# Optimization experiments

Measured on AMD Instinct MI355X. Metric: run time of the kernel, lower is better.

## Reference

```python
import jax, jax.numpy as jnp
import numpy as np

N, E, G, H = 25000, 400000, 64, 8


def setup_inputs() -> dict:
    key = jax.random.key(0)
    ks = iter(jax.random.split(key, 64))
    nrm = lambda *s: jax.random.normal(next(ks), s, dtype=jnp.float32) * 0.1
    inp = {}
    inp['x'] = jax.random.normal(next(ks), (N, 3), dtype=jnp.float32)
    inp['edge_index'] = jax.random.randint(next(ks), (2, E), 0, N)
    inp['edge_attr'] = jax.random.uniform(next(ks), (E, 1), dtype=jnp.float32)
    inp['batch'] = jnp.sort(jax.random.randint(next(ks), (N,), 0, G))
    inp['inbn_g'] = jnp.ones(3, jnp.float32); inp['inbn_b'] = jnp.zeros(3, jnp.float32)
    # GAT layer 0: in=3, heads=8, C=8, concat -> 64
    inp['w0'] = nrm(3, 64); inp['we0'] = nrm(1, 64)
    inp['as0'] = nrm(8, 8); inp['ad0'] = nrm(8, 8); inp['ae0'] = nrm(8, 8)
    inp['b0'] = jnp.zeros(64, jnp.float32)
    inp['bng0'] = jnp.ones(64, jnp.float32); inp['bnb0'] = jnp.zeros(64, jnp.float32)
    # GAT layer 1: in=64, heads=8, C=8, concat -> 64
    inp['w1'] = nrm(64, 64); inp['we1'] = nrm(1, 64)
    inp['as1'] = nrm(8, 8); inp['ad1'] = nrm(8, 8); inp['ae1'] = nrm(8, 8)
    inp['b1'] = jnp.zeros(64, jnp.float32)
    inp['bng1'] = jnp.ones(64, jnp.float32); inp['bnb1'] = jnp.zeros(64, jnp.float32)
    # GAT layer 2: in=64, heads=8, C=64, concat=False (mean over heads) -> 64
    inp['w2'] = nrm(64, 512); inp['we2'] = nrm(1, 512)
    inp['as2'] = nrm(8, 64); inp['ad2'] = nrm(8, 64); inp['ae2'] = nrm(8, 64)
    inp['b2'] = jnp.zeros(64, jnp.float32)
    inp['bng2'] = jnp.ones(64, jnp.float32); inp['bnb2'] = jnp.zeros(64, jnp.float32)
    # MLP head (weights stored [in, out])
    inp['fc1_w'] = nrm(128, 128); inp['fc1_b'] = jnp.zeros(128, jnp.float32)
    inp['fc2_w'] = nrm(128, 64); inp['fc2_b'] = jnp.zeros(64, jnp.float32)
    inp['fg_w'] = nrm(64, 1); inp['fg_b'] = jnp.zeros(1, jnp.float32)
    inp['fb_w'] = nrm(64, 1); inp['fb_b'] = jnp.zeros(1, jnp.float32)
    return inp


def _bn(x, g, b):
    # training-mode batch norm over node dim (biased variance)
    m = x.mean(0)
    v = jnp.mean((x - m) ** 2, 0)
    return (x - m) * jax.lax.rsqrt(v + 1e-5) * g + b


def _gat(x, ei, ea, W, We, a_s, a_d, a_e, bias, concat):
    n = x.shape[0]
    h, c = a_s.shape
    xs = (x @ W).reshape(n, h, c)                       # [N,H,C]
    asrc = jnp.einsum('nhc,hc->nh', xs, a_s)            # [N,H]
    adst = jnp.einsum('nhc,hc->nh', xs, a_d)
    ee = (ea @ We).reshape(-1, h, c)                    # [E,H,C]
    aedge = jnp.einsum('ehc,hc->eh', ee, a_e)           # [E,H]
    s, d = ei[0], ei[1]
    logit = jax.nn.leaky_relu(asrc[s] + adst[d] + aedge, 0.2)   # [E,H]
    # segment softmax over incoming edges of each destination node
    mx = jax.ops.segment_max(logit, d, num_segments=n)
    mx = jnp.where(jnp.isfinite(mx), mx, 0.0)
    ez = jnp.exp(logit - mx[d])
    den = jax.ops.segment_sum(ez, d, num_segments=n)
    alpha = ez / jnp.maximum(den[d], 1e-16)             # [E,H]
    out = jax.ops.segment_sum(alpha[:, :, None] * xs[s], d, num_segments=n)  # [N,H,C]
    out = out.reshape(n, h * c) if concat else out.mean(1)
    return out + bias


def reference(x, edge_index, edge_attr, batch, inbn_g, inbn_b,
              w0, we0, as0, ad0, ae0, b0, bng0, bnb0,
              w1, we1, as1, ad1, ae1, b1, bng1, bnb1,
              w2, we2, as2, ad2, ae2, b2, bng2, bnb2,
              fc1_w, fc1_b, fc2_w, fc2_b, fg_w, fg_b, fb_w, fb_b):
    x = _bn(x, inbn_g, inbn_b)
    # layer 0 (no residual: 3 != 64)
    x = jax.nn.elu(_bn(_gat(x, edge_index, edge_attr, w0, we0, as0, ad0, ae0, b0, True), bng0, bnb0))
    # layer 1 (residual)
    x = x + jax.nn.elu(_bn(_gat(x, edge_index, edge_attr, w1, we1, as1, ad1, ae1, b1, True), bng1, bnb1))
    # layer 2 (concat=False, residual)
    x = x + jax.nn.elu(_bn(_gat(x, edge_index, edge_attr, w2, we2, as2, ad2, ae2, b2, False), bng2, bnb2))
    # dual pooling per graph
    cnt = jax.ops.segment_sum(jnp.ones((x.shape[0],), x.dtype), batch, num_segments=G)
    x_mean = jax.ops.segment_sum(x, batch, num_segments=G) / jnp.maximum(cnt, 1.0)[:, None]
    x_max = jax.ops.segment_max(x, batch, num_segments=G)
    g = jnp.concatenate([x_mean, x_max], axis=1)        # [G,128]
    g = jax.nn.elu(g @ fc1_w + fc1_b)
    g = jax.nn.elu(g @ fc2_w + fc2_b)
    gamma = g @ fg_w + fg_b
    beta = g @ fb_w + fb_b
    return jnp.concatenate([gamma, beta], axis=1)       # [G, 2*p_layers]
```

## Files before the change

### kernel.cpp

```cpp
#include <hip/hip_runtime.h>
#include <math.h>

#define NN 25000
#define EE 400000
#define GG 64

static const int O_DEG   = 0;
static const int ZERO_END= 25000;
static const int O_ROWS  = 25008;
static const int O_CUR   = 50016;
static const int O_GOFF  = 75016;
static const int O_IPART = 75088;
static const int O_INBN  = 75184;
static const int O_WS    = 75192;
static const int O_WD    = 76728;
static const int O_WE    = 78264;
static const int O_BPART = 78288;
static const int O_AB    = 94672;
static const int O_BSW   = 94800;
static const int O_CSRC  = 111184;
static const int O_CEA   = 511184;
static const int O_XS    = 911184;
static const int O_ASRC  = 2511184;
static const int O_ADST  = 2711184;
static const int O_AGG   = 2911184;
static const int O_X     = 4511184;
static const int O_BSWC  = 6111184;
static const int O_BSWA  = 6113744;
static const int O_BSUM  = 6114256;
static const int O_BOFF  = 6114360;

using f32x4 = __attribute__((ext_vector_type(4))) float;
using sh8   = __attribute__((ext_vector_type(8))) short;

__device__ inline short f2bf(float f) {
    unsigned u = __float_as_uint(f);
    unsigned r = (u + 0x7FFFu + ((u >> 16) & 1u)) >> 16;
    return (short)r;
}

__global__ void k_pre(const int* __restrict__ ei, const int* __restrict__ batch,
                      const float* __restrict__ x3,
                      const float* w0, const float* we0, const float* as0, const float* ad0, const float* ae0,
                      const float* w1, const float* we1, const float* as1, const float* ad1, const float* ae1,
                      const float* w2, const float* we2, const float* as2, const float* ad2, const float* ae2,
                      int* __restrict__ deg, int* __restrict__ goff, float* __restrict__ ipart,
                      float* __restrict__ Ws, float* __restrict__ Wd, float* __restrict__ wev,
                      short* __restrict__ bsw, short* __restrict__ bswc, short* __restrict__ bswa) {
    __shared__ float sd[1536];
    int b = blockIdx.x, t = threadIdx.x;
    if (b < 1563) {
        int e = b * 256 + t;
        if (e < EE) atomicAdd(&deg[ei[EE + e]], 1);
    } else if (b < 1579) {
        int ib = b - 1563;
        float s[3] = {0,0,0}, q[3] = {0,0,0};
        for (int n = ib * 256 + t; n < NN; n += 16 * 256) {
#pragma unroll
            for (int i = 0; i < 3; i++) { float v = x3[n*3+i]; s[i] += v; q[i] += v*v; }
        }
#pragma unroll
        for (int i = 0; i < 3; i++) { sd[t*6+i] = s[i]; sd[t*6+3+i] = q[i]; }
        __syncthreads();
        for (int off = 128; off > 0; off >>= 1) {
            if (t < off) {
#pragma unroll
                for (int i = 0; i < 6; i++) sd[t*6+i] += sd[(t+off)*6+i];
            }
            __syncthreads();
        }
        if (t < 6) ipart[ib*6 + t] = sd[t];
    } else if (b == 1579) {
        if (t <= GG) {
            int g = t, lo = 0, hi = NN;
            while (lo < hi) { int mid = (lo + hi) >> 1; if (batch[mid] < g) lo = mid + 1; else hi = mid; }
            goff[g] = lo;
        }
    } else if (b < 1583) {
        int L = b - 1580;
        const float *W, *Wep, *as_, *ad_, *ae_; int INF, CC;
        if (L == 0)      { W = w0; Wep = we0; as_ = as0; ad_ = ad0; ae_ = ae0; INF = 3;  CC = 8;  }
        else if (L == 1) { W = w1; Wep = we1; as_ = as1; ad_ = ad1; ae_ = ae1; INF = 64; CC = 8;  }
        else             { W = w2; Wep = we2; as_ = as2; ad_ = ad2; ae_ = ae2; INF = 64; CC = 64; }
        int HC = 8 * CC;
        for (int tt = t; tt < INF * 8; tt += 256) {
            int i = tt >> 3, h = tt & 7;
            float s = 0.f, d = 0.f;
            for (int c = 0; c < CC; c++) {
                float w = W[i*HC + h*CC + c];
                s += w * as_[h*CC + c];
                d += w * ad_[h*CC + c];
            }
            Ws[L*512 + i*8 + h] = s; Wd[L*512 + i*8 + h] = d;
        }
        if (t < 8) {
            float s = 0.f;
            for (int c = 0; c < CC; c++) s += Wep[t*CC + c] * ae_[t*CC + c];
            wev[L*8 + t] = s;
        }
    } else if (b < 1711) {
        int idx = (b - 1583) * 256 + t;
        int j  = idx & 7;
        int l  = (idx >> 3) & 63;
        int nt = (idx >> 9) & 3;
        int kb = idx >> 11;
        int k = kb*32 + (l >> 4)*4 + (j & 3) + 16*(j >> 2);
        int c = nt*16 + (l & 15);
        int h = k >> 6, i = k & 63;
        bsw[idx] = f2bf(w2[i*512 + h*64 + c]);
    } else if (b < 1731) {
        int idx = (b - 1711) * 256 + t;
        int j  = idx & 7;
        int l  = (idx >> 3) & 63;
        int r2 = idx >> 9;
        int nt = r2 % 5, kb = r2 / 5;
        int k = kb*32 + (l >> 4)*4 + (j & 3) + 16*(j >> 2);
        int c = nt*16 + (l & 15);
        float val;
        if (c < 64) val = w1[k*64 + c];
        else {
            int h = (c - 64) & 7;
            const float* aa = (c < 72) ? as1 : ad1;
            float s = 0.f;
            for (int cc = 0; cc < 8; cc++) s += w1[k*64 + h*8 + cc] * aa[h*8 + cc];
            val = s;
        }
        bswc[idx] = f2bf(val);
    } else {
        int idx = (b - 1731) * 256 + t;
        int j  = idx & 7;
        int l  = (idx >> 3) & 63;
        int kb = idx >> 9;
        int k = kb*32 + (l >> 4)*4 + (j & 3) + 16*(j >> 2);
        int c = l & 15;
        int h = c & 7;
        const float* aa = (c < 8) ? as2 : ad2;
        float s = 0.f;
        for (int cc = 0; cc < 64; cc++) s += w2[k*512 + h*64 + cc] * aa[h*64 + cc];
        bswa[idx] = f2bf(s);
    }
}

__global__ void k_scan1(const int* __restrict__ deg, int* __restrict__ rows,
                        int* __restrict__ bsum) {
    int t = threadIdx.x, b = blockIdx.x;
    int i = b * 256 + t;
    int v = (i < NN) ? deg[i] : 0;
    __shared__ int sd[256];
    sd[t] = v; __syncthreads();
    for (int off = 1; off < 256; off <<= 1) {
        int x = (t >= off) ? sd[t - off] : 0;
        __syncthreads();
        sd[t] += x;
        __syncthreads();
    }
    if (i < NN) rows[i] = sd[t] - v;
    if (t == 255) bsum[b] = sd[255];
}

__global__ void k_scan2(const int* __restrict__ bsum, int* __restrict__ boff,
                        const float* __restrict__ ipart, float* __restrict__ inbn) {
    int t = threadIdx.x;
    if (t == 0) {
        int run = 0;
        for (int b = 0; b < 98; b++) { int v = bsum[b]; boff[b] = run; run += v; }
    }
    if (t < 6) { float s = 0.f; for (int b = 0; b < 16; b++) s += ipart[b*6 + t]; inbn[t] = s; }
}

__global__ void k_scan3(const int* __restrict__ boff, int* __restrict__ rows,
                        int* __restrict__ cur) {
    int t = threadIdx.x, b = blockIdx.x;
    int i = b * 256 + t;
    if (i < NN) {
        int r = rows[i] + boff[b];
        rows[i] = r;
        cur[i] = r;
    }
    if (b == 0 && t == 0) rows[NN] = EE;
}

__global__ void k_fill(const int* __restrict__ ei, const float* __restrict__ ea,
                       int* __restrict__ cur, int* __restrict__ csrc,
                       float* __restrict__ cea) {
    int e = blockIdx.x * 256 + threadIdx.x;
    if (e >= EE) return;
    int s = ei[e], d = ei[EE + e];
    int pos = atomicAdd(&cur[d], 1);
    csrc[pos] = s; cea[pos] = ea[e];
}

__global__ void k_proj0(const float* __restrict__ x, const float* __restrict__ sums,
                        const float* __restrict__ g, const float* __restrict__ b,
                        const float* __restrict__ W0,
                        const float* __restrict__ Ws, const float* __restrict__ Wd,
                        float* __restrict__ xs, float* __restrict__ asrc, float* __restrict__ adst) {
    int idx = blockIdx.x * 256 + threadIdx.x;
    if (idx >= NN * 64) return;
    int n = idx >> 6, j = idx & 63;
    float xn[3];
#pragma unroll
    for (int i = 0; i < 3; i++) {
        float m = sums[i] * (1.0f / NN);
        float v = sums[3+i] * (1.0f / NN) - m*m;
        xn[i] = (x[n*3+i] - m) * rsqrtf(v + 1e-5f) * g[i] + b[i];
    }
    float a = 0.f;
#pragma unroll
    for (int i = 0; i < 3; i++) a += xn[i] * W0[i*64 + j];
    xs[n*64 + j] = a;
    if (j < 16) {
        const float* WA = (j < 8) ? Ws : Wd;
        int h = j & 7;
        float s = 0.f;
#pragma unroll
        for (int i = 0; i < 3; i++) s += xn[i] * WA[i*8 + h];
        if (j < 8) asrc[n*8 + h] = s; else adst[n*8 + h] = s;
    }
}

__global__ void k_agg8f(const int* __restrict__ rows, const int* __restrict__ csrc,
                        const float* __restrict__ cea,
                        const float* __restrict__ asrc, const float* __restrict__ adst,
                        const float* __restrict__ wev,
                        const float* __restrict__ xs, float* __restrict__ agg) {
    int lane = threadIdx.x & 63;
    int d = (blockIdx.x * blockDim.x + threadIdx.x) >> 6;
    if (d >= NN) return;
    int h = lane >> 3;
    float adh = adst[d*8 + h];
    float wh  = wev[h];
    int rs = rows[d], re = rows[d+1];
    float acc = 0.f, den = 0.f;
    for (int c0 = rs; c0 < re; c0 += 64) {
        int cnt = re - c0; if (cnt > 64) cnt = 64;
        int ii = c0 + (lane < cnt ? lane : 0);
        int es = csrc[ii];
        float ef = cea[ii];
        int j = 0;
        for (; j + 3 < cnt; j += 4) {
            int s0 = __shfl(es, j),   s1 = __shfl(es, j+1);
            int s2 = __shfl(es, j+2), s3 = __shfl(es, j+3);
            float a0 = __shfl(ef, j),   a1 = __shfl(ef, j+1);
            float a2 = __shfl(ef, j+2), a3 = __shfl(ef, j+3);
            float l0 = asrc[s0*8+h], l1 = asrc[s1*8+h];
            float l2 = asrc[s2*8+h], l3 = asrc[s3*8+h];
            float x0 = xs[s0*64+lane], x1 = xs[s1*64+lane];
            float x2 = xs[s2*64+lane], x3 = xs[s3*64+lane];
            l0 += adh + a0*wh; l1 += adh + a1*wh;
            l2 += adh + a2*wh; l3 += adh + a3*wh;
            l0 = fmaxf(l0, 0.2f*l0); l1 = fmaxf(l1, 0.2f*l1);
            l2 = fmaxf(l2, 0.2f*l2); l3 = fmaxf(l3, 0.2f*l3);
            float e0 = __expf(l0), e1 = __expf(l1), e2 = __expf(l2), e3 = __expf(l3);
            den += (e0 + e1) + (e2 + e3);
            acc += e0*x0; acc += e1*x1; acc += e2*x2; acc += e3*x3;
        }
        for (; j < cnt; j++) {
            int s = __shfl(es, j);
            float a = __shfl(ef, j);
            float l = asrc[s*8+h] + adh + a*wh;
            l = fmaxf(l, 0.2f*l);
            float e = __expf(l);
            den += e;
            acc += e * xs[s*64+lane];
        }
    }
    agg[d*64 + lane] = acc / fmaxf(den, 1e-16f);
}

__global__ void k_proj1m(const float* __restrict__ agg, const float* __restrict__ ab,
                         const short* __restrict__ bswc,
                         float* __restrict__ xb, float* __restrict__ xs,
                         float* __restrict__ asrc, float* __restrict__ adst) {
    int l = threadIdx.x & 63;
    int wid = (blockIdx.x * blockDim.x + threadIdx.x) >> 6;
    int n0 = wid * 16;
    if (n0 >= NN) return;
    int ra = n0 + (l & 15); if (ra > NN-1) ra = NN-1;
    int kq = (l >> 4) * 4;
    const sh8* Bs = (const sh8*)bswc;
    sh8 af0, af1;
#pragma unroll
    for (int kb = 0; kb < 2; kb++) {
        int c0 = kb*32 + kq;
        float4 a0 = *(const float4*)&agg[ra*64 + c0];
        float4 a1 = *(const float4*)&agg[ra*64 + c0 + 16];
        float4 sc0 = *(const float4*)&ab[c0];
        float4 sh0 = *(const float4*)&ab[64 + c0];
        float4 sc1 = *(const float4*)&ab[c0 + 16];
        float4 sh1 = *(const float4*)&ab[64 + c0 + 16];
        float o[8];
        o[0] = a0.x*sc0.x + sh0.x; o[1] = a0.y*sc0.y + sh0.y;
        o[2] = a0.z*sc0.z + sh0.z; o[3] = a0.w*sc0.w + sh0.w;
        o[4] = a1.x*sc1.x + sh1.x; o[5] = a1.y*sc1.y + sh1.y;
        o[6] = a1.z*sc1.z + sh1.z; o[7] = a1.w*sc1.w + sh1.w;
#pragma unroll
        for (int u = 0; u < 8; u++) o[u] = (o[u] > 0.f) ? o[u] : (__expf(o[u]) - 1.f);
        float4 w0v = {o[0],o[1],o[2],o[3]}, w1v = {o[4],o[5],o[6],o[7]};
        *(float4*)&xb[ra*64 + c0]      = w0v;
        *(float4*)&xb[ra*64 + c0 + 16] = w1v;
        sh8 af;
#pragma unroll
        for (int u = 0; u < 8; u++) af[u] = f2bf(o[u]);
        if (kb == 0) af0 = af; else af1 = af;
    }
    f32x4 acc[5];
#pragma unroll
    for (int nt = 0; nt < 5; nt++) acc[nt] = (f32x4){0,0,0,0};
#pragma unroll
    for (int nt = 0; nt < 5; nt++) {
        acc[nt] = __builtin_amdgcn_mfma_f32_16x16x32_bf16(af0, Bs[nt*64 + l], acc[nt], 0, 0, 0);
        acc[nt] = __builtin_amdgcn_mfma_f32_16x16x32_bf16(af1, Bs[(5+nt)*64 + l], acc[nt], 0, 0, 0);
    }
    int rbase = n0 + (l >> 4) * 4, cb = l & 15;
#pragma unroll
    for (int r = 0; r < 4; r++) {
        int n = rbase + r;
        if (n >= NN) break;
#pragma unroll
        for (int nt = 0; nt < 4; nt++) xs[n*64 + nt*16 + cb] = acc[nt][r];
        if (cb < 8) asrc[n*8 + cb] = acc[4][r];
        else        adst[n*8 + (cb-8)] = acc[4][r];
    }
}

__global__ void k_bnattn(const float* __restrict__ agg, const float* __restrict__ ab,
                         const short* __restrict__ bswa,
                         float* __restrict__ xb,
                         float* __restrict__ asrc, float* __restrict__ adst) {
    int l = threadIdx.x & 63;
    int wid = (blockIdx.x * blockDim.x + threadIdx.x) >> 6;
    int n0 = wid * 16;
    if (n0 >= NN) return;
    int ra = n0 + (l & 15); if (ra > NN-1) ra = NN-1;
    int kq = (l >> 4) * 4;
    const sh8* Bs = (const sh8*)bswa;
    sh8 af0, af1;
#pragma unroll
    for (int kb = 0; kb < 2; kb++) {
        int c0 = kb*32 + kq;
        float4 a0 = *(const float4*)&agg[ra*64 + c0];
        float4 a1 = *(const float4*)&agg[ra*64 + c0 + 16];
        float4 x0 = *(const float4*)&xb[ra*64 + c0];
        float4 x1 = *(const float4*)&xb[ra*64 + c0 + 16];
        float4 sc0 = *(const float4*)&ab[c0];
        float4 sh0 = *(const float4*)&ab[64 + c0];
        float4 sc1 = *(const float4*)&ab[c0 + 16];
        float4 sh1 = *(const float4*)&ab[64 + c0 + 16];
        float o[8];
        o[0] = a0.x*sc0.x + sh0.x; o[1] = a0.y*sc0.y + sh0.y;
        o[2] = a0.z*sc0.z + sh0.z; o[3] = a0.w*sc0.w + sh0.w;
        o[4] = a1.x*sc1.x + sh1.x; o[5] = a1.y*sc1.y + sh1.y;
        o[6] = a1.z*sc1.z + sh1.z; o[7] = a1.w*sc1.w + sh1.w;
#pragma unroll
        for (int u = 0; u < 8; u++) o[u] = (o[u] > 0.f) ? o[u] : (__expf(o[u]) - 1.f);
        o[0] += x0.x; o[1] += x0.y; o[2] += x0.z; o[3] += x0.w;
        o[4] += x1.x; o[5] += x1.y; o[6] += x1.z; o[7] += x1.w;
        float4 w0v = {o[0],o[1],o[2],o[3]}, w1v = {o[4],o[5],o[6],o[7]};
        *(float4*)&xb[ra*64 + c0]      = w0v;
        *(float4*)&xb[ra*64 + c0 + 16] = w1v;
        sh8 af;
#pragma unroll
        for (int u = 0; u < 8; u++) af[u] = f2bf(o[u]);
        if (kb == 0) af0 = af; else af1 = af;
    }
    f32x4 acc = {0,0,0,0};
    acc = __builtin_amdgcn_mfma_f32_16x16x32_bf16(af0, Bs[l],      acc, 0, 0, 0);
    acc = __builtin_amdgcn_mfma_f32_16x16x32_bf16(af1, Bs[64 + l], acc, 0, 0, 0);
    int rbase = n0 + (l >> 4) * 4, cb = l & 15;
#pragma unroll
    for (int r = 0; r < 4; r++) {
        int n = rbase + r;
        if (n >= NN) break;
        if (cb < 8) asrc[n*8 + cb] = acc[r];
        else        adst[n*8 + (cb-8)] = acc[r];
    }
}

__global__ __launch_bounds__(256) void k_l2f(
        const int* __restrict__ rows, const int* __restrict__ csrc,
        const float* __restrict__ cea,
        const float* __restrict__ asrc, const float* __restrict__ adst,
        const float* __restrict__ wev,
        const float* __restrict__ x, const short* __restrict__ bsw,
        float* __restrict__ agg) {
    __shared__ short zl[16 * 520];
    int t = threadIdx.x, lane = t & 63, wv = t >> 6;
    int blk = blockIdx.x;
    int h = lane >> 3;
    float wh = wev[h];
    const float4* x4 = (const float4*)x;
    int fo   = (lane & 7) * 2;
    int kb_w = lane >> 2;
    int qd0  = 2 * (lane & 1);
    int jhi  = 4 * ((lane >> 1) & 1);
    for (int q = 0; q < 4; q++) {
        int r = wv * 4 + q;
        int d = blk * 16 + r;
        float acc[8] = {0,0,0,0,0,0,0,0};
        float den = 0.f;
        if (d < NN) {
            float adh = adst[d*8 + h];
            int rs = rows[d], re = rows[d+1];
            for (int c0 = rs; c0 < re; c0 += 64) {
                int cnt = re - c0; if (cnt > 64) cnt = 64;
                int ii = c0 + (lane < cnt ? lane : 0);
                int es = csrc[ii];
                float ef = cea[ii];
                int j = 0;
                for (; j + 1 < cnt; j += 2) {
                    int s0 = __shfl(es, j), s1 = __shfl(es, j+1);
                    float a0 = __shfl(ef, j), a1 = __shfl(ef, j+1);
                    float l0 = asrc[s0*8+h], l1 = asrc[s1*8+h];
                    float4 u0 = x4[s0*16 + fo], u1 = x4[s0*16 + fo + 1];
                    float4 v0 = x4[s1*16 + fo], v1 = x4[s1*16 + fo + 1];
                    l0 += adh + a0*wh; l1 += adh + a1*wh;
                    l0 = fmaxf(l0, 0.2f*l0); l1 = fmaxf(l1, 0.2f*l1);
                    float e0 = __expf(l0), e1 = __expf(l1);
                    den += e0 + e1;
                    acc[0] += e0*u0.x + e1*v0.x;
                    acc[1] += e0*u0.y + e1*v0.y;
                    acc[2] += e0*u0.z + e1*v0.z;
                    acc[3] += e0*u0.w + e1*v0.w;
                    acc[4] += e0*u1.x + e1*v1.x;
                    acc[5] += e0*u1.y + e1*v1.y;
                    acc[6] += e0*u1.z + e1*v1.z;
                    acc[7] += e0*u1.w + e1*v1.w;
                }
                if (j < cnt) {
                    int s = __shfl(es, j);
                    float a = __shfl(ef, j);
                    float l = asrc[s*8+h] + adh + a*wh;
                    l = fmaxf(l, 0.2f*l);
                    float e = __expf(l);
                    den += e;
                    float4 u0 = x4[s*16 + fo], u1 = x4[s*16 + fo + 1];
                    acc[0] += e*u0.x; acc[1] += e*u0.y; acc[2] += e*u0.z; acc[3] += e*u0.w;
                    acc[4] += e*u1.x; acc[5] += e*u1.y; acc[6] += e*u1.z; acc[7] += e*u1.w;
                }
            }
        }
        float inv = 1.0f / fmaxf(den, 1e-16f);
        short4 lo, hi;
        lo.x = f2bf(acc[0]*inv); lo.y = f2bf(acc[1]*inv);
        lo.z = f2bf(acc[2]*inv); lo.w = f2bf(acc[3]*inv);
        hi.x = f2bf(acc[4]*inv); hi.y = f2bf(acc[5]*inv);
        hi.z = f2bf(acc[6]*inv); hi.w = f2bf(acc[7]*inv);
        *(short4*)&zl[kb_w*520 + (r + 16*qd0)*8 + jhi]     = lo;
        *(short4*)&zl[kb_w*520 + (r + 16*(qd0+1))*8 + jhi] = hi;
    }
    __syncthreads();
    const sh8* Bs = (const sh8*)bsw;
    f32x4 acc = {0,0,0,0};
    for (int kb = 0; kb < 16; kb++) {
        sh8 a = *(const sh8*)&zl[kb*520 + lane*8];
        sh8 bf = Bs[(kb*4 + wv)*64 + lane];
        acc = __builtin_amdgcn_mfma_f32_16x16x32_bf16(a, bf, acc, 0, 0, 0);
    }
    int row = blk*16 + (lane >> 4) * 4;
    int col = wv*16 + (lane & 15);
#pragma unroll
    for (int rr = 0; rr < 4; rr++) {
        int n = row + rr;
        if (n < NN) agg[(size_t)n*64 + col] = acc[rr] * 0.125f;
    }
}

__global__ void k_bnstats(const float* __restrict__ agg, float* __restrict__ part) {
    int t = threadIdx.x;
    int c = t & 63;
    int r0 = blockIdx.x * 4 + (t >> 6);
    float s = 0.f, q = 0.f;
    for (int n = r0; n < NN; n += gridDim.x * 4) {
        float y = agg[n*64 + c];
        s += y; q += y*y;
    }
    __shared__ float sd[512];
    sd[t] = s; sd[256 + t] = q;
    __syncthreads();
    if (t < 128) { sd[t] += sd[t+128]; sd[256+t] += sd[256+t+128]; }
    __syncthreads();
    if (t < 64) {
        part[blockIdx.x*128 + t]      = sd[t] + sd[t+64];
        part[blockIdx.x*128 + 64 + t] = sd[256+t] + sd[256+t+64];
    }
}

__global__ void k_bnfin(const float* __restrict__ part, const float* __restrict__ gam,
                        const float* __restrict__ bet, float* __restrict__ ab) {
    int c = threadIdx.x;
    if (c >= 64) return;
    float s = 0.f, q = 0.f;
    for (int b = 0; b < 128; b++) { s += part[b*128 + c]; q += part[b*128 + 64 + c]; }
    float m = s * (1.0f / NN);
    float v = q * (1.0f / NN) - m*m;
    float a = gam[c] * rsqrtf(v + 1e-5f);
    ab[c] = a;
    ab[64 + c] = bet[c] - m * a;
}

__global__ void k_poolmlp(const float* __restrict__ xb, const float* __restrict__ agg,
                          const float* __restrict__ ab, const int* __restrict__ goff,
                          const float* __restrict__ fc1w, const float* __restrict__ fc1b,
                          const float* __restrict__ fc2w, const float* __restrict__ fc2b,
                          const float* __restrict__ fgw, const float* __restrict__ fgb,
                          const float* __restrict__ fbw, const float* __restrict__ fbb,
                          float* __restrict__ out) {
    int g = blockIdx.x, t = threadIdx.x;
    int c = t & 63, r = t >> 6;
    float a = ab[c], sh = ab[64 + c];
    int st = goff[g], en = goff[g+1];
    float s = 0.f, mx = -INFINITY;
    for (int n = st + r; n < en; n += 4) {
        float o = agg[n*64 + c] * a + sh;
        o = (o > 0.f) ? o : (__expf(o) - 1.0f);
        float v = xb[n*64 + c] + o;
        s += v; mx = fmaxf(mx, v);
    }
    __shared__ float sd[512];
    __shared__ float sg[128], s1[128], s2[64];
    sd[t] = s; sd[256 + t] = mx;
    __syncthreads();
    if (t < 128) { sd[t] += sd[t+128]; sd[256+t] = fmaxf(sd[256+t], sd[256+t+128]); }
    __syncthreads();
    if (t < 64) {
        float cnt = (float)(en - st);
        sg[t]      = (sd[t] + sd[t+64]) / fmaxf(cnt, 1.0f);
        sg[64 + t] = fmaxf(sd[256+t], sd[256+t+64]);
    }
    __syncthreads();
    if (t < 128) {
        float av = fc1b[t];
        for (int i = 0; i < 128; i++) av += sg[i] * fc1w[i*128 + t];
        s1[t] = (av > 0.f) ? av : (__expf(av) - 1.f);
    }
    __syncthreads();
    if (t < 64) {
        float bv = fc2b[t];
        for (int i = 0; i < 128; i++) bv += s1[i] * fc2w[i*64 + t];
        s2[t] = (bv > 0.f) ? bv : (__expf(bv) - 1.f);
    }
    __syncthreads();
    if (t == 0) {
        float ga = fgb[0], be = fbb[0];
        for (int i = 0; i < 64; i++) { ga += s2[i] * fgw[i]; be += s2[i] * fbw[i]; }
        out[g*2 + 0] = ga;
        out[g*2 + 1] = be;
    }
}

extern "C" void kernel_launch(void* const* d_in, const int* in_sizes, int n_in,
                              void* d_out, int out_size, void* d_ws, size_t ws_size,
                              hipStream_t stream) {
    (void)in_sizes; (void)n_in; (void)out_size; (void)ws_size;
    const float* x3    = (const float*)d_in[0];
    const int*   ei    = (const int*)d_in[1];
    const float* ea    = (const float*)d_in[2];
    const int*   batch = (const int*)d_in[3];
    const float* ing   = (const float*)d_in[4];
    const float* inb   = (const float*)d_in[5];
    const float* w0    = (const float*)d_in[6];
    const float* we0   = (const float*)d_in[7];
    const float* as0   = (const float*)d_in[8];
    const float* ad0   = (const float*)d_in[9];
    const float* ae0   = (const float*)d_in[10];
    const float* bng0  = (const float*)d_in[12];
    const float* bnb0  = (const float*)d_in[13];
    const float* w1    = (const float*)d_in[14];
    const float* we1   = (const float*)d_in[15];
    const float* as1   = (const float*)d_in[16];
    const float* ad1   = (const float*)d_in[17];
    const float* ae1   = (const float*)d_in[18];
    const float* bng1  = (const float*)d_in[20];
    const float* bnb1  = (const float*)d_in[21];
    const float* w2    = (const float*)d_in[22];
    const float* we2   = (const float*)d_in[23];
    const float* as2   = (const float*)d_in[24];
    const float* ad2   = (const float*)d_in[25];
    const float* ae2   = (const float*)d_in[26];
    const float* bng2  = (const float*)d_in[28];
    const float* bnb2  = (const float*)d_in[29];
    const float* fc1w  = (const float*)d_in[30];
    const float* fc1b  = (const float*)d_in[31];
    const float* fc2w  = (const float*)d_in[32];
    const float* fc2b  = (const float*)d_in[33];
    const float* fgw   = (const float*)d_in[34];
    const float* fgb   = (const float*)d_in[35];
    const float* fbw   = (const float*)d_in[36];
    const float* fbb   = (const float*)d_in[37];

    float* fws = (float*)d_ws;
    int*   iws = (int*)d_ws;
    int*   deg   = iws + O_DEG;
    int*   rows  = iws + O_ROWS;
    int*   cur   = iws + O_CUR;
    int*   goff  = iws + O_GOFF;
    float* ipart = fws + O_IPART;
    float* inbn  = fws + O_INBN;
    float* Ws    = fws + O_WS;
    float* Wd    = fws + O_WD;
    float* wev   = fws + O_WE;
    float* bpart = fws + O_BPART;
    float* ab    = fws + O_AB;
    short* bsw   = (short*)(fws + O_BSW);
    int*   csrc  = iws + O_CSRC;
    float* cea   = fws + O_CEA;
    float* xs    = fws + O_XS;
    float* asrc  = fws + O_ASRC;
    float* adst  = fws + O_ADST;
    float* agg   = fws + O_AGG;
    float* xb    = fws + O_X;
    short* bswc  = (short*)(fws + O_BSWC);
    short* bswa  = (short*)(fws + O_BSWA);
    int*   bsum  = iws + O_BSUM;
    int*   boff  = iws + O_BOFF;

    hipMemsetAsync(d_ws, 0, (size_t)ZERO_END * sizeof(int), stream);

    k_pre<<<1735, 256, 0, stream>>>(ei, batch, x3,
                                    w0, we0, as0, ad0, ae0,
                                    w1, we1, as1, ad1, ae1,
                                    w2, we2, as2, ad2, ae2,
                                    deg, goff, ipart, Ws, Wd, wev, bsw, bswc, bswa);
    k_scan1<<<98, 256, 0, stream>>>(deg, rows, bsum);
    k_scan2<<<1, 64, 0, stream>>>(bsum, boff, ipart, inbn);
    k_scan3<<<98, 256, 0, stream>>>(boff, rows, cur);
    k_fill<<<(EE + 255) / 256, 256, 0, stream>>>(ei, ea, cur, csrc, cea);

    const int nblk64 = (NN * 64 + 255) / 256;
    const int wblk16 = ((NN + 15) / 16 + 3) / 4;

    k_proj0<<<nblk64, 256, 0, stream>>>(x3, inbn, ing, inb, w0, Ws, Wd, xs, asrc, adst);
    k_agg8f<<<nblk64, 256, 0, stream>>>(rows, csrc, cea, asrc, adst, wev, xs, agg);
    k_bnstats<<<128, 256, 0, stream>>>(agg, bpart);
    k_bnfin<<<1, 64, 0, stream>>>(bpart, bng0, bnb0, ab);

    k_proj1m<<<wblk16, 256, 0, stream>>>(agg, ab, bswc, xb, xs, asrc, adst);
    k_agg8f<<<nblk64, 256, 0, stream>>>(rows, csrc, cea, asrc, adst, wev + 8, xs, agg);
    k_bnstats<<<128, 256, 0, stream>>>(agg, bpart);
    k_bnfin<<<1, 64, 0, stream>>>(bpart, bng1, bnb1, ab);

    k_bnattn<<<wblk16, 256, 0, stream>>>(agg, ab, bswa, xb, asrc, adst);
    k_l2f<<<(NN + 15) / 16, 256, 0, stream>>>(rows, csrc, cea, asrc, adst, wev + 16,
                                              xb, bsw, agg);
    k_bnstats<<<128, 256, 0, stream>>>(agg, bpart);
    k_bnfin<<<1, 64, 0, stream>>>(bpart, bng2, bnb2, ab);

    k_poolmlp<<<GG, 256, 0, stream>>>(xb, agg, ab, goff, fc1w, fc1b, fc2w, fc2b,
                                      fgw, fgb, fbw, fbb, (float*)d_out);
}
```

Before: 419.8 us.

## Build CSR with per-block LDS histograms instead of global atomics

Replaces the global-atomic degree count and fill with 64 blocks that each histogram a fixed edge slice in LDS (about 100 KB of shared memory). A two-level scan then gives each block its own per-destination cursors, and the fill pass bumps those cursors with LDS atomics. This removes global atomic contention and the memset, and makes the CSR order deterministic. In exchange, only 64 blocks run with a large LDS footprint, and the scans now read 64x more count data.

```diff
diff --git a/kernel.cpp b/kernel.cpp
--- a/kernel.cpp
+++ b/kernel.cpp
@@ -4,31 +4,33 @@
 #define NN 25000
 #define EE 400000
 #define GG 64
-
-static const int O_DEG   = 0;
-static const int ZERO_END= 25000;
-static const int O_ROWS  = 25008;
-static const int O_CUR   = 50016;
-static const int O_GOFF  = 75016;
-static const int O_IPART = 75088;
-static const int O_INBN  = 75184;
-static const int O_WS    = 75192;
-static const int O_WD    = 76728;
-static const int O_WE    = 78264;
-static const int O_BPART = 78288;
-static const int O_AB    = 94672;
-static const int O_BSW   = 94800;
-static const int O_CSRC  = 111184;
-static const int O_CEA   = 511184;
-static const int O_XS    = 911184;
-static const int O_ASRC  = 2511184;
-static const int O_ADST  = 2711184;
-static const int O_AGG   = 2911184;
-static const int O_X     = 4511184;
-static const int O_BSWC  = 6111184;
-static const int O_BSWA  = 6113744;
-static const int O_BSUM  = 6114256;
-static const int O_BOFF  = 6114360;
+#define NB 64
+#define PL 25024
+#define EPB 6250
+
+static const int O_CNT   = 0;
+static const int O_ROWS  = 1601536;
+static const int O_CUR   = 1626544;
+static const int O_GOFF  = 3228080;
+static const int O_IPART = 3228152;
+static const int O_INBN  = 3228248;
+static const int O_WS    = 3228256;
+static const int O_WD    = 3229792;
+static const int O_WE    = 3231328;
+static const int O_BPART = 3231360;
+static const int O_AB    = 3247744;
+static const int O_BSW   = 3247872;
+static const int O_CSRC  = 3264256;
+static const int O_CEA   = 3664256;
+static const int O_XS    = 4064256;
+static const int O_ASRC  = 5664256;
+static const int O_ADST  = 5864256;
+static const int O_AGG   = 6064256;
+static const int O_X     = 7664256;
+static const int O_BSWC  = 9264256;
+static const int O_BSWA  = 9266816;
+static const int O_BSUM  = 9267328;
+static const int O_BOFF  = 9267432;
 
 using f32x4 = __attribute__((ext_vector_type(4))) float;
 using sh8   = __attribute__((ext_vector_type(8))) short;
@@ -39,21 +41,17 @@
     return (short)r;
 }
 
-__global__ void k_pre(const int* __restrict__ ei, const int* __restrict__ batch,
-                      const float* __restrict__ x3,
+__global__ void k_pre(const int* __restrict__ batch, const float* __restrict__ x3,
                       const float* w0, const float* we0, const float* as0, const float* ad0, const float* ae0,
                       const float* w1, const float* we1, const float* as1, const float* ad1, const float* ae1,
                       const float* w2, const float* we2, const float* as2, const float* ad2, const float* ae2,
-                      int* __restrict__ deg, int* __restrict__ goff, float* __restrict__ ipart,
+                      int* __restrict__ goff, float* __restrict__ ipart,
                       float* __restrict__ Ws, float* __restrict__ Wd, float* __restrict__ wev,
                       short* __restrict__ bsw, short* __restrict__ bswc, short* __restrict__ bswa) {
     __shared__ float sd[1536];
     int b = blockIdx.x, t = threadIdx.x;
-    if (b < 1563) {
-        int e = b * 256 + t;
-        if (e < EE) atomicAdd(&deg[ei[EE + e]], 1);
-    } else if (b < 1579) {
-        int ib = b - 1563;
+    if (b < 16) {
+        int ib = b;
         float s[3] = {0,0,0}, q[3] = {0,0,0};
         for (int n = ib * 256 + t; n < NN; n += 16 * 256) {
 #pragma unroll
@@ -70,14 +68,14 @@
             __syncthreads();
         }
         if (t < 6) ipart[ib*6 + t] = sd[t];
-    } else if (b == 1579) {
+    } else if (b == 16) {
         if (t <= GG) {
             int g = t, lo = 0, hi = NN;
             while (lo < hi) { int mid = (lo + hi) >> 1; if (batch[mid] < g) lo = mid + 1; else hi = mid; }
             goff[g] = lo;
         }
-    } else if (b < 1583) {
-        int L = b - 1580;
+    } else if (b < 20) {
+        int L = b - 17;
         const float *W, *Wep, *as_, *ad_, *ae_; int INF, CC;
         if (L == 0)      { W = w0; Wep = we0; as_ = as0; ad_ = ad0; ae_ = ae0; INF = 3;  CC = 8;  }
         else if (L == 1) { W = w1; Wep = we1; as_ = as1; ad_ = ad1; ae_ = ae1; INF = 64; CC = 8;  }
@@ -98,8 +96,8 @@
             for (int c = 0; c < CC; c++) s += Wep[t*CC + c] * ae_[t*CC + c];
             wev[L*8 + t] = s;
         }
-    } else if (b < 1711) {
-        int idx = (b - 1583) * 256 + t;
+    } else if (b < 148) {
+        int idx = (b - 20) * 256 + t;
         int j  = idx & 7;
         int l  = (idx >> 3) & 63;
         int nt = (idx >> 9) & 3;
@@ -108,8 +106,8 @@
         int c = nt*16 + (l & 15);
         int h = k >> 6, i = k & 63;
         bsw[idx] = f2bf(w2[i*512 + h*64 + c]);
-    } else if (b < 1731) {
-        int idx = (b - 1711) * 256 + t;
+    } else if (b < 168) {
+        int idx = (b - 148) * 256 + t;
         int j  = idx & 7;
         int l  = (idx >> 3) & 63;
         int r2 = idx >> 9;
@@ -127,7 +125,7 @@
         }
         bswc[idx] = f2bf(val);
     } else {
-        int idx = (b - 1731) * 256 + t;
+        int idx = (b - 168) * 256 + t;
         int j  = idx & 7;
         int l  = (idx >> 3) & 63;
         int kb = idx >> 9;
@@ -141,11 +139,26 @@
     }
 }
 
-__global__ void k_scan1(const int* __restrict__ deg, int* __restrict__ rows,
+__global__ __launch_bounds__(256) void k_hist(const int* __restrict__ ei, int* __restrict__ cnt) {
+    __shared__ int hb[PL];
+    int t = threadIdx.x, b = blockIdx.x;
+    for (int i = t; i < PL; i += 256) hb[i] = 0;
+    __syncthreads();
+    int e0 = b * EPB;
+    for (int e = e0 + t; e < e0 + EPB; e += 256)
+        atomicAdd(&hb[ei[EE + e]], 1);
+    __syncthreads();
+    for (int i = t; i < NN; i += 256) cnt[b * PL + i] = hb[i];
+}
+
+__global__ void k_scan1(const int* __restrict__ cnt, int* __restrict__ rows,
                         int* __restrict__ bsum) {
     int t = threadIdx.x, b = blockIdx.x;
     int i = b * 256 + t;
-    int v = (i < NN) ? deg[i] : 0;
+    int v = 0;
+    if (i < NN) {
+        for (int r = 0; r < NB; r++) v += cnt[r * PL + i];
+    }
     __shared__ int sd[256];
     sd[t] = v; __syncthreads();
     for (int off = 1; off < 256; off <<= 1) {
@@ -168,26 +181,34 @@
     if (t < 6) { float s = 0.f; for (int b = 0; b < 16; b++) s += ipart[b*6 + t]; inbn[t] = s; }
 }
 
-__global__ void k_scan3(const int* __restrict__ boff, int* __restrict__ rows,
-                        int* __restrict__ cur) {
+__global__ void k_scan3(const int* __restrict__ boff, const int* __restrict__ cnt,
+                        int* __restrict__ rows, int* __restrict__ cur) {
     int t = threadIdx.x, b = blockIdx.x;
     int i = b * 256 + t;
     if (i < NN) {
-        int r = rows[i] + boff[b];
-        rows[i] = r;
-        cur[i] = r;
+        int run = rows[i] + boff[b];
+        rows[i] = run;
+        for (int r = 0; r < NB; r++) {
+            cur[r * PL + i] = run;
+            run += cnt[r * PL + i];
+        }
     }
     if (b == 0 && t == 0) rows[NN] = EE;
 }
 
-__global__ void k_fill(const int* __restrict__ ei, const float* __restrict__ ea,
-                       int* __restrict__ cur, int* __restrict__ csrc,
+__global__ __launch_bounds__(256) void k_fill(const int* __restrict__ ei, const float* __restrict__ ea,
+                       const int* __restrict__ cur, int* __restrict__ csrc,
                        float* __restrict__ cea) {
-    int e = blockIdx.x * 256 + threadIdx.x;
-    if (e >= EE) return;
-    int s = ei[e], d = ei[EE + e];
-    int pos = atomicAdd(&cur[d], 1);
-    csrc[pos] = s; cea[pos] = ea[e];
+    __shared__ int lc[PL];
+    int t = threadIdx.x, b = blockIdx.x;
+    for (int i = t; i < NN; i += 256) lc[i] = cur[b * PL + i];
+    __syncthreads();
+    int e0 = b * EPB;
+    for (int e = e0 + t; e < e0 + EPB; e += 256) {
+        int s = ei[e], d = ei[EE + e];
+        int pos = atomicAdd(&lc[d], 1);
+        csrc[pos] = s; cea[pos] = ea[e];
+    }
 }
 
 __global__ void k_proj0(const float* __restrict__ x, const float* __restrict__ sums,
@@ -591,7 +612,7 @@
 
     float* fws = (float*)d_ws;
     int*   iws = (int*)d_ws;
-    int*   deg   = iws + O_DEG;
+    int*   cnt   = iws + O_CNT;
     int*   rows  = iws + O_ROWS;
     int*   cur   = iws + O_CUR;
     int*   goff  = iws + O_GOFF;
@@ -615,17 +636,16 @@
     int*   bsum  = iws + O_BSUM;
     int*   boff  = iws + O_BOFF;
 
-    hipMemsetAsync(d_ws, 0, (size_t)ZERO_END * sizeof(int), stream);
-
-    k_pre<<<1735, 256, 0, stream>>>(ei, batch, x3,
-                                    w0, we0, as0, ad0, ae0,
-                                    w1, we1, as1, ad1, ae1,
-                                    w2, we2, as2, ad2, ae2,
-                                    deg, goff, ipart, Ws, Wd, wev, bsw, bswc, bswa);
-    k_scan1<<<98, 256, 0, stream>>>(deg, rows, bsum);
+    k_pre<<<172, 256, 0, stream>>>(batch, x3,
+                                   w0, we0, as0, ad0, ae0,
+                                   w1, we1, as1, ad1, ae1,
+                                   w2, we2, as2, ad2, ae2,
+                                   goff, ipart, Ws, Wd, wev, bsw, bswc, bswa);
+    k_hist<<<NB, 256, 0, stream>>>(ei, cnt);
+    k_scan1<<<98, 256, 0, stream>>>(cnt, rows, bsum);
     k_scan2<<<1, 64, 0, stream>>>(bsum, boff, ipart, inbn);
-    k_scan3<<<98, 256, 0, stream>>>(boff, rows, cur);
-    k_fill<<<(EE + 255) / 256, 256, 0, stream>>>(ei, ea, cur, csrc, cea);
+    k_scan3<<<98, 256, 0, stream>>>(boff, cnt, rows, cur);
+    k_fill<<<NB, 256, 0, stream>>>(ei, ea, cur, csrc, cea);
 
     const int nblk64 = (NN * 64 + 255) / 256;
     const int wblk16 = ((NN + 15) / 16 + 3) / 4;
```

After: 416.5 us. Within noise of the previous version (-0.8%).
